# Kernel tuning notes

Measured on AMD Instinct MI355X. Metric: run time of the kernel, lower is better.

The kernel has to match this reference:

```python
import jax, jax.numpy as jnp
import numpy as np

DIN, HID = 256, 512
SCALE = 1.0 / (64.0 * 6.0 ** 2)  # q / 2304, as in the torch code
NEG = 9e15


def setup_inputs() -> dict:
    key = jax.random.key(0)
    ks = jax.random.split(key, 8)
    B, N = 32, 1024
    x = jax.random.normal(ks[0], (B, N, DIN), dtype=jnp.float32)
    mask = jax.random.randint(ks[1], (B, N, N), 0, 2).astype(jnp.float32)
    lim = 1.0 / np.sqrt(DIN)
    Wv = jax.random.uniform(ks[2], (DIN, HID), minval=-lim, maxval=lim, dtype=jnp.float32)
    bv = jax.random.uniform(ks[3], (HID,), minval=-lim, maxval=lim, dtype=jnp.float32)
    Wk = jax.random.uniform(ks[4], (DIN, HID), minval=-lim, maxval=lim, dtype=jnp.float32)
    bk = jax.random.uniform(ks[5], (HID,), minval=-lim, maxval=lim, dtype=jnp.float32)
    Wq = jax.random.uniform(ks[6], (DIN, HID), minval=-lim, maxval=lim, dtype=jnp.float32)
    bq = jax.random.uniform(ks[7], (HID,), minval=-lim, maxval=lim, dtype=jnp.float32)
    return {"x": x, "mask": mask, "Wv": Wv, "bv": bv, "Wk": Wk, "bk": bk, "Wq": Wq, "bq": bq}


def reference(x, mask, Wv, bv, Wk, bk, Wq, bq):
    v = jax.nn.relu(x @ Wv + bv)                      # [B,N,H]
    q = jax.nn.relu(x @ Wq + bq)                      # [B,N,H]
    k = jax.nn.relu(x @ Wk + bk)                      # [B,N,H]
    scores = jnp.einsum('bnh,bmh->bnm', q * SCALE, k)  # [B,N,N]
    att = jax.nn.softmax(scores * mask - NEG * (1.0 - mask), axis=2)
    out = jax.nn.relu(jnp.einsum('bnm,bmh->bnh', att, v))
    return out
```

## Files before the change

kernel.cpp:

```cpp
#include <hip/hip_runtime.h>
#include <hip/hip_bf16.h>

#define DIN   256
#define HID   512
#define NBAT  32
#define NSEQ  1024
#define SCALEF (1.0f / 2304.0f)
#define NEGC  9e15f

typedef __attribute__((ext_vector_type(4))) float f32x4;
typedef __attribute__((ext_vector_type(8))) short bf16x8;
typedef unsigned short u16;

__device__ __forceinline__ u16 f2bf(float f) {
    union { float f; unsigned u; } v; v.f = f;
    unsigned r = v.u + 0x7fffu + ((v.u >> 16) & 1u);
    return (u16)(r >> 16);
}

__device__ __forceinline__ float bf2f(u16 b) {
    union { unsigned u; float f; } v; v.u = ((unsigned)b) << 16;
    return v.f;
}

__device__ __forceinline__ void g2lds16(const void* g, void* l) {
    __builtin_amdgcn_global_load_lds(
        (const __attribute__((address_space(1))) void*)g,
        (__attribute__((address_space(3))) void*)l,
        16, 0, 0);
}

__global__ __launch_bounds__(256) void prep_x(const float* __restrict__ x,
                                              u16* __restrict__ xb) {
    long i = (long)blockIdx.x * 256 + threadIdx.x;
    const long n4 = (long)NBAT * NSEQ * DIN / 4;
    if (i < n4) {
        float4 v = ((const float4*)x)[i];
        ushort4 o;
        o.x = f2bf(v.x); o.y = f2bf(v.y); o.z = f2bf(v.z); o.w = f2bf(v.w);
        ((ushort4*)xb)[i] = o;
    }
}

__global__ __launch_bounds__(256) void prep_w(
    const float* __restrict__ Wv, const float* __restrict__ bv,
    const float* __restrict__ Wk, const float* __restrict__ bk,
    const float* __restrict__ Wq, const float* __restrict__ bq,
    u16* __restrict__ Wtb, float* __restrict__ biascat) {
    int i = blockIdx.x * 256 + threadIdx.x;
    if (i < 1536 * 256) {
        int n = i >> 8, k = i & 255;
        const float* W = (n < 512) ? Wv : ((n < 1024) ? Wk : Wq);
        Wtb[i] = f2bf(W[k * 512 + (n & 511)]);
    }
    if (i < 1536) {
        biascat[i] = (i < 512) ? bv[i] : ((i < 1024) ? bk[i - 512] : bq[i - 1024]);
    }
}

template<int EPI>
__global__ __launch_bounds__(256) void gemm128(
    const u16* __restrict__ A, int lda, long sA,
    const u16* __restrict__ Bt, int ldb, long sB,
    void* __restrict__ Cv, int ldc, long sC,
    int K, const float* __restrict__ bias) {
    __shared__ u16 lA[128 * 32];
    __shared__ u16 lB[128 * 32];
    const int t = threadIdx.x;
    const int lane = t & 63;
    const int w = t >> 6;
    const int b = blockIdx.z;
    const u16* Ab = A + (long)b * sA;
    const u16* Bb = Bt + (long)b * sB;
    const int bm = blockIdx.x * 128, bn = blockIdx.y * 128;

    const int srow = t >> 2;
    const int soff = (t & 3) * 8;
    const u16* gA0 = Ab + (long)(bm + srow) * lda + soff;
    const u16* gA1 = Ab + (long)(bm + srow + 64) * lda + soff;
    const u16* gB0 = Bb + (long)(bn + srow) * ldb + soff;
    const u16* gB1 = Bb + (long)(bn + srow + 64) * ldb + soff;

    const int wr = (w >> 1) * 64, wc = (w & 1) * 64;
    const int frow = lane & 15, fk = (lane >> 4) * 8;

    f32x4 acc[4][4] = {};

    for (int k0 = 0; k0 < K; k0 += 32) {
        __syncthreads();
        g2lds16(gA0 + k0, &lA[t * 8]);
        g2lds16(gA1 + k0, &lA[2048 + t * 8]);
        g2lds16(gB0 + k0, &lB[t * 8]);
        g2lds16(gB1 + k0, &lB[2048 + t * 8]);
        __syncthreads();

        bf16x8 af[4], bfr[4];
#pragma unroll
        for (int i = 0; i < 4; ++i)
            af[i] = *(const bf16x8*)&lA[(wr + i * 16 + frow) * 32 + fk];
#pragma unroll
        for (int j = 0; j < 4; ++j)
            bfr[j] = *(const bf16x8*)&lB[(wc + j * 16 + frow) * 32 + fk];
#pragma unroll
        for (int i = 0; i < 4; ++i)
#pragma unroll
            for (int j = 0; j < 4; ++j)
                acc[i][j] = __builtin_amdgcn_mfma_f32_16x16x32_bf16(
                    af[i], bfr[j], acc[i][j], 0, 0, 0);
    }

    const int crow0 = bm + wr + (lane >> 4) * 4;
    const int ccol0 = bn + wc + (lane & 15);
#pragma unroll
    for (int i = 0; i < 4; ++i) {
#pragma unroll
        for (int j = 0; j < 4; ++j) {
            int col = ccol0 + j * 16;
#pragma unroll
            for (int r = 0; r < 4; ++r) {
                int row = crow0 + i * 16 + r;
                float v = acc[i][j][r];
                if (EPI == 0) {
                    v += bias[col];
                    v = v > 0.0f ? v : 0.0f;
                    if (col >= 1024) v *= SCALEF;
                    ((u16*)Cv)[(long)b * sC + (long)row * ldc + col] = f2bf(v);
                } else if (EPI == 1) {
                    ((u16*)Cv)[(long)b * sC + (long)row * ldc + col] = f2bf(v);
                } else {
                    ((float*)Cv)[(long)b * sC + (long)row * ldc + col] =
                        v > 0.0f ? v : 0.0f;
                }
            }
        }
    }
}

__global__ __launch_bounds__(256) void transpose_v(const u16* __restrict__ qkv,
                                                   u16* __restrict__ vt) {
    __shared__ u16 tile[64][72];
    const int t = threadIdx.x;
    const int b = blockIdx.z;
    const int n0 = blockIdx.x * 64, h0 = blockIdx.y * 64;
    const u16* src = qkv + (long)(b * NSEQ + n0) * 1536 + h0;
#pragma unroll
    for (int it = 0; it < 2; ++it) {
        int n = (t >> 3) + it * 32;
        int hc = (t & 7) * 8;
        *(bf16x8*)&tile[n][hc] = *(const bf16x8*)&src[(long)n * 1536 + hc];
    }
    __syncthreads();
    u16* dst = vt + ((long)b * HID + h0) * NSEQ + n0;
#pragma unroll
    for (int it = 0; it < 2; ++it) {
        int h = (t >> 3) + it * 32;
        int nc = (t & 7) * 8;
        bf16x8 v;
#pragma unroll
        for (int j = 0; j < 8; ++j) v[j] = (short)tile[nc + j][h];
        *(bf16x8*)&dst[(long)h * NSEQ + nc] = v;
    }
}

__global__ __launch_bounds__(256) void softmax_mask(
    const u16* __restrict__ S, const float* __restrict__ mask,
    u16* __restrict__ P) {
    const long row = blockIdx.x;
    const int t = threadIdx.x;
    ushort4 sv = ((const ushort4*)(S + row * NSEQ))[t];
    float4 mv = ((const float4*)(mask + row * NSEQ))[t];
    float l0 = mv.x * bf2f(sv.x) - NEGC * (1.0f - mv.x);
    float l1 = mv.y * bf2f(sv.y) - NEGC * (1.0f - mv.y);
    float l2 = mv.z * bf2f(sv.z) - NEGC * (1.0f - mv.z);
    float l3 = mv.w * bf2f(sv.w) - NEGC * (1.0f - mv.w);

    float mx = fmaxf(fmaxf(l0, l1), fmaxf(l2, l3));
#pragma unroll
    for (int off = 32; off; off >>= 1) mx = fmaxf(mx, __shfl_xor(mx, off));
    __shared__ float redm[4];
    if ((t & 63) == 0) redm[t >> 6] = mx;
    __syncthreads();
    mx = fmaxf(fmaxf(redm[0], redm[1]), fmaxf(redm[2], redm[3]));

    float e0 = __expf(l0 - mx), e1 = __expf(l1 - mx);
    float e2 = __expf(l2 - mx), e3 = __expf(l3 - mx);
    float sum = (e0 + e1) + (e2 + e3);
#pragma unroll
    for (int off = 32; off; off >>= 1) sum += __shfl_xor(sum, off);
    __shared__ float reds[4];
    if ((t & 63) == 0) reds[t >> 6] = sum;
    __syncthreads();
    sum = (reds[0] + reds[1]) + (reds[2] + reds[3]);

    float inv = 1.0f / sum;
    ushort4 o;
    o.x = f2bf(e0 * inv); o.y = f2bf(e1 * inv);
    o.z = f2bf(e2 * inv); o.w = f2bf(e3 * inv);
    ((ushort4*)(P + row * NSEQ))[t] = o;
}

extern "C" void kernel_launch(void* const* d_in, const int* in_sizes, int n_in,
                              void* d_out, int out_size, void* d_ws, size_t ws_size,
                              hipStream_t stream) {
    const float* x    = (const float*)d_in[0];
    const float* mask = (const float*)d_in[1];
    const float* Wv   = (const float*)d_in[2];
    const float* bv   = (const float*)d_in[3];
    const float* Wk   = (const float*)d_in[4];
    const float* bk   = (const float*)d_in[5];
    const float* Wq   = (const float*)d_in[6];
    const float* bq   = (const float*)d_in[7];
    float* out = (float*)d_out;

    char* ws = (char*)d_ws;
    u16*   xb      = (u16*)ws;   ws += (long)NBAT * NSEQ * DIN * 2;
    u16*   Wtb     = (u16*)ws;   ws += (long)1536 * 256 * 2;
    float* biascat = (float*)ws; ws += 1536 * 4;
    u16*   qkv     = (u16*)ws;   ws += (long)NBAT * NSEQ * 1536 * 2;
    u16*   vt      = (u16*)ws;   ws += (long)NBAT * HID * NSEQ * 2;

    size_t used = (size_t)(ws - (char*)d_ws);
    size_t rem = (ws_size > used) ? ws_size - used : 0;
    int CH = 1;
    for (int c = 32; c >= 1; c >>= 1) {
        if ((size_t)c * NSEQ * NSEQ * 4 <= rem) { CH = c; break; }
    }
    u16* S = (u16*)ws;           ws += (long)CH * NSEQ * NSEQ * 2;
    u16* P = (u16*)ws;           ws += (long)CH * NSEQ * NSEQ * 2;

    prep_x<<<8192, 256, 0, stream>>>(x, xb);
    prep_w<<<1536, 256, 0, stream>>>(Wv, bv, Wk, bk, Wq, bq, Wtb, biascat);

    gemm128<0><<<dim3(256, 12, 1), 256, 0, stream>>>(
        xb, 256, 0L, Wtb, 256, 0L, qkv, 1536, 0L, 256, biascat);

    transpose_v<<<dim3(16, 8, NBAT), 256, 0, stream>>>(qkv, vt);

    const long sQKV = (long)NSEQ * 1536;
    for (int c = 0; c < NBAT / CH; ++c) {
        const u16* qb = qkv + (long)c * CH * sQKV + 1024;
        const u16* kb = qkv + (long)c * CH * sQKV + 512;
        gemm128<1><<<dim3(8, 8, CH), 256, 0, stream>>>(
            qb, 1536, sQKV, kb, 1536, sQKV, S, NSEQ, (long)NSEQ * NSEQ, 512, nullptr);
        softmax_mask<<<CH * NSEQ, 256, 0, stream>>>(
            S, mask + (long)c * CH * NSEQ * NSEQ, P);
        gemm128<2><<<dim3(8, 4, CH), 256, 0, stream>>>(
            P, NSEQ, (long)NSEQ * NSEQ, vt, NSEQ, (long)HID * NSEQ,
            out + (long)c * CH * NSEQ * HID, HID, (long)NSEQ * HID, NSEQ, nullptr);
    }
}
```

Baseline: 445.9 us.

## Process all batches at once with in-place softmax, swizzled grids, and smaller PV tiles

Removes the workspace-dependent batch chunking and gives S/P one shared buffer that the softmax overwrites in place, so the pipeline runs in three launches instead of a per-chunk loop. Adds a block-index swizzle that interleaves batches across consecutive workgroups (likely to spread work across XCDs and help cache locality). Makes the PV GEMM use 64-row tiles so it launches more blocks. It needs a full-size 64 MB score buffer, which the workspace may not hold, and the smaller tiles reuse data less.

```diff
diff --git a/kernel.cpp b/kernel.cpp
--- a/kernel.cpp
+++ b/kernel.cpp
@@ -58,21 +58,33 @@
     }
 }
 
-template<int EPI>
-__global__ __launch_bounds__(256) void gemm128(
+template<int EPI, int BM, int SWZ>
+__global__ __launch_bounds__(256) void gemm_t(
     const u16* __restrict__ A, int lda, long sA,
     const u16* __restrict__ Bt, int ldb, long sB,
     void* __restrict__ Cv, int ldc, long sC,
-    int K, const float* __restrict__ bias) {
-    __shared__ u16 lA[128 * 32];
+    int K, const float* __restrict__ bias, int gx, int gy) {
+    __shared__ u16 lA[BM * 32];
     __shared__ u16 lB[128 * 32];
     const int t = threadIdx.x;
     const int lane = t & 63;
     const int w = t >> 6;
-    const int b = blockIdx.z;
+
+    int b, bxi, byi;
+    if (SWZ) {
+        int f = (int)blockIdx.x;
+        int per = gx * gy;
+        int j = f >> 3;
+        b = (f & 7) + 8 * (j / per);
+        int r = j % per;
+        bxi = r % gx; byi = r / gx;
+    } else {
+        b = blockIdx.z; bxi = blockIdx.x; byi = blockIdx.y;
+    }
+
     const u16* Ab = A + (long)b * sA;
     const u16* Bb = Bt + (long)b * sB;
-    const int bm = blockIdx.x * 128, bn = blockIdx.y * 128;
+    const int bm = bxi * BM, bn = byi * 128;
 
     const int srow = t >> 2;
     const int soff = (t & 3) * 8;
@@ -81,30 +93,32 @@
     const u16* gB0 = Bb + (long)(bn + srow) * ldb + soff;
     const u16* gB1 = Bb + (long)(bn + srow + 64) * ldb + soff;
 
-    const int wr = (w >> 1) * 64, wc = (w & 1) * 64;
+    constexpr int NJ = (BM == 128) ? 4 : 2;
+    const int wr = (BM == 128) ? (w >> 1) * 64 : 0;
+    const int wc = (BM == 128) ? (w & 1) * 64 : w * 32;
     const int frow = lane & 15, fk = (lane >> 4) * 8;
 
-    f32x4 acc[4][4] = {};
+    f32x4 acc[4][NJ] = {};
 
     for (int k0 = 0; k0 < K; k0 += 32) {
         __syncthreads();
         g2lds16(gA0 + k0, &lA[t * 8]);
-        g2lds16(gA1 + k0, &lA[2048 + t * 8]);
+        if (BM == 128) g2lds16(gA1 + k0, &lA[2048 + t * 8]);
         g2lds16(gB0 + k0, &lB[t * 8]);
         g2lds16(gB1 + k0, &lB[2048 + t * 8]);
         __syncthreads();
 
-        bf16x8 af[4], bfr[4];
+        bf16x8 af[4], bfr[NJ];
 #pragma unroll
         for (int i = 0; i < 4; ++i)
             af[i] = *(const bf16x8*)&lA[(wr + i * 16 + frow) * 32 + fk];
 #pragma unroll
-        for (int j = 0; j < 4; ++j)
+        for (int j = 0; j < NJ; ++j)
             bfr[j] = *(const bf16x8*)&lB[(wc + j * 16 + frow) * 32 + fk];
 #pragma unroll
         for (int i = 0; i < 4; ++i)
 #pragma unroll
-            for (int j = 0; j < 4; ++j)
+            for (int j = 0; j < NJ; ++j)
                 acc[i][j] = __builtin_amdgcn_mfma_f32_16x16x32_bf16(
                     af[i], bfr[j], acc[i][j], 0, 0, 0);
     }
@@ -114,7 +128,7 @@
 #pragma unroll
     for (int i = 0; i < 4; ++i) {
 #pragma unroll
-        for (int j = 0; j < 4; ++j) {
+        for (int j = 0; j < NJ; ++j) {
             int col = ccol0 + j * 16;
 #pragma unroll
             for (int r = 0; r < 4; ++r) {
@@ -163,11 +177,10 @@
 }
 
 __global__ __launch_bounds__(256) void softmax_mask(
-    const u16* __restrict__ S, const float* __restrict__ mask,
-    u16* __restrict__ P) {
+    u16* __restrict__ SP, const float* __restrict__ mask) {
     const long row = blockIdx.x;
     const int t = threadIdx.x;
-    ushort4 sv = ((const ushort4*)(S + row * NSEQ))[t];
+    ushort4 sv = ((const ushort4*)(SP + row * NSEQ))[t];
     float4 mv = ((const float4*)(mask + row * NSEQ))[t];
     float l0 = mv.x * bf2f(sv.x) - NEGC * (1.0f - mv.x);
     float l1 = mv.y * bf2f(sv.y) - NEGC * (1.0f - mv.y);
@@ -196,7 +209,7 @@
     ushort4 o;
     o.x = f2bf(e0 * inv); o.y = f2bf(e1 * inv);
     o.z = f2bf(e2 * inv); o.w = f2bf(e3 * inv);
-    ((ushort4*)(P + row * NSEQ))[t] = o;
+    ((ushort4*)(SP + row * NSEQ))[t] = o;
 }
 
 extern "C" void kernel_launch(void* const* d_in, const int* in_sizes, int n_in,
@@ -218,34 +231,24 @@
     float* biascat = (float*)ws; ws += 1536 * 4;
     u16*   qkv     = (u16*)ws;   ws += (long)NBAT * NSEQ * 1536 * 2;
     u16*   vt      = (u16*)ws;   ws += (long)NBAT * HID * NSEQ * 2;
-
-    size_t used = (size_t)(ws - (char*)d_ws);
-    size_t rem = (ws_size > used) ? ws_size - used : 0;
-    int CH = 1;
-    for (int c = 32; c >= 1; c >>= 1) {
-        if ((size_t)c * NSEQ * NSEQ * 4 <= rem) { CH = c; break; }
-    }
-    u16* S = (u16*)ws;           ws += (long)CH * NSEQ * NSEQ * 2;
-    u16* P = (u16*)ws;           ws += (long)CH * NSEQ * NSEQ * 2;
+    u16*   SP      = (u16*)ws;   ws += (long)NBAT * NSEQ * NSEQ * 2;
 
     prep_x<<<8192, 256, 0, stream>>>(x, xb);
     prep_w<<<1536, 256, 0, stream>>>(Wv, bv, Wk, bk, Wq, bq, Wtb, biascat);
 
-    gemm128<0><<<dim3(256, 12, 1), 256, 0, stream>>>(
-        xb, 256, 0L, Wtb, 256, 0L, qkv, 1536, 0L, 256, biascat);
+    gemm_t<0, 128, 0><<<dim3(256, 12, 1), 256, 0, stream>>>(
+        xb, 256, 0L, Wtb, 256, 0L, qkv, 1536, 0L, 256, biascat, 0, 0);
 
     transpose_v<<<dim3(16, 8, NBAT), 256, 0, stream>>>(qkv, vt);
 
     const long sQKV = (long)NSEQ * 1536;
-    for (int c = 0; c < NBAT / CH; ++c) {
-        const u16* qb = qkv + (long)c * CH * sQKV + 1024;
-        const u16* kb = qkv + (long)c * CH * sQKV + 512;
-        gemm128<1><<<dim3(8, 8, CH), 256, 0, stream>>>(
-            qb, 1536, sQKV, kb, 1536, sQKV, S, NSEQ, (long)NSEQ * NSEQ, 512, nullptr);
-        softmax_mask<<<CH * NSEQ, 256, 0, stream>>>(
-            S, mask + (long)c * CH * NSEQ * NSEQ, P);
-        gemm128<2><<<dim3(8, 4, CH), 256, 0, stream>>>(
-            P, NSEQ, (long)NSEQ * NSEQ, vt, NSEQ, (long)HID * NSEQ,
-            out + (long)c * CH * NSEQ * HID, HID, (long)NSEQ * HID, NSEQ, nullptr);
-    }
-}
+    gemm_t<1, 128, 1><<<NBAT * 8 * 8, 256, 0, stream>>>(
+        qkv + 1024, 1536, sQKV, qkv + 512, 1536, sQKV,
+        SP, NSEQ, (long)NSEQ * NSEQ, 512, nullptr, 8, 8);
+
+    softmax_mask<<<NBAT * NSEQ, 256, 0, stream>>>(SP, mask);
+
+    gemm_t<2, 64, 1><<<NBAT * 16 * 4, 256, 0, stream>>>(
+        SP, NSEQ, (long)NSEQ * NSEQ, vt, NSEQ, (long)HID * NSEQ,
+        out, HID, (long)NSEQ * HID, NSEQ, nullptr, 16, 4);
+}
```

After: 426.5 us. 4.3% less time.
